# Kernel optimization log

Measured on AMD Instinct MI355X. Metric: run time of the kernel, lower is better.

The kernel has to match this reference:

```python
import jax, jax.numpy as jnp
import numpy as np

NEG_SLOPE = 0.2
EPS = 1e-16


def _gat_layer(x, src, dst, W, a_src, a_dst, b, n_nodes):
    # x: [N, Fin], W: [Fout, Fin]; src/dst: [E'] (self-loops already appended)
    h = x @ W.T                              # [N, Fout]
    alpha_s = h @ a_src                      # [N] per-source score
    alpha_d = h @ a_dst                      # [N] per-dest score
    e = jax.nn.leaky_relu(alpha_s[src] + alpha_d[dst], NEG_SLOPE)  # [E']
    # segment softmax over destination nodes (PyG softmax semantics)
    m = jax.ops.segment_max(e, dst, num_segments=n_nodes)          # [N]
    ex = jnp.exp(e - m[dst])                                       # [E']
    s = jax.ops.segment_sum(ex, dst, num_segments=n_nodes)         # [N]
    alpha = ex / (s[dst] + EPS)                                    # [E']
    out = jax.ops.segment_sum(alpha[:, None] * h[src], dst, num_segments=n_nodes)
    return out + b, alpha


def setup_inputs() -> dict:
    key = jax.random.key(0)
    ks = jax.random.split(key, 14)
    N, E, F_IN, H1, H2, F_OUT = 50000, 800000, 128, 64, 64, 32
    sc = 0.1
    return {
        "x": jax.random.normal(ks[0], (N, F_IN), dtype=jnp.float32),
        "edge_index": jax.random.randint(ks[1], (2, E), 0, N, dtype=jnp.int64),
        "W1": jax.random.normal(ks[2], (H1, F_IN), dtype=jnp.float32) * sc,
        "a_src1": jax.random.normal(ks[3], (H1,), dtype=jnp.float32) * sc,
        "a_dst1": jax.random.normal(ks[4], (H1,), dtype=jnp.float32) * sc,
        "b1": jnp.zeros((H1,), dtype=jnp.float32),
        "W2": jax.random.normal(ks[5], (H2, H1), dtype=jnp.float32) * sc,
        "a_src2": jax.random.normal(ks[6], (H2,), dtype=jnp.float32) * sc,
        "a_dst2": jax.random.normal(ks[7], (H2,), dtype=jnp.float32) * sc,
        "b2": jnp.zeros((H2,), dtype=jnp.float32),
        "W3": jax.random.normal(ks[8], (F_OUT, H2), dtype=jnp.float32) * sc,
        "a_src3": jax.random.normal(ks[9], (F_OUT,), dtype=jnp.float32) * sc,
        "a_dst3": jax.random.normal(ks[10], (F_OUT,), dtype=jnp.float32) * sc,
        "b3": jnp.zeros((F_OUT,), dtype=jnp.float32),
    }


def reference(x, edge_index, W1, a_src1, a_dst1, b1, W2, a_src2, a_dst2, b2, W3, a_src3, a_dst3, b3):
    N = x.shape[0]
    loops = jnp.arange(N, dtype=edge_index.dtype)
    src = jnp.concatenate([edge_index[0], loops])  # add_self_loops=True
    dst = jnp.concatenate([edge_index[1], loops])

    h, alpha1 = _gat_layer(x, src, dst, W1, a_src1, a_dst1, b1, N)
    h = jax.nn.relu(h)
    h, _ = _gat_layer(h, src, dst, W2, a_src2, a_dst2, b2, N)
    h = jax.nn.relu(h)
    out, _ = _gat_layer(h, src, dst, W3, a_src3, a_dst3, b3, N)
    # att_tuple = (edge_index with self loops, attention coefficients of layer 1)
    return (jnp.stack([src, dst]), alpha1, out)
```

## Files before the change

kernel.cpp:

```cpp
#include <hip/hip_runtime.h>
#include <hip/hip_bf16.h>
#include <math.h>

#define NEG_SLOPE 0.2f
#define GAT_EPS 1e-16f

constexpr int NN = 50000;
constexpr int NE = 800000;
constexpr int EP = NE + NN;
constexpr int NB = (NN + 255) / 256;

__device__ inline void edge_sd(const int* __restrict__ ei, int i, int& s, int& d) {
    if (i < NE) { s = ei[i]; d = ei[NE + i]; }
    else        { s = d = i - NE; }
}

__device__ inline float bflo(unsigned int h) { return __uint_as_float(h << 16); }
__device__ inline float bfhi(unsigned int h) { return __uint_as_float(h & 0xffff0000u); }

__global__ void k_edges_hist(const int* __restrict__ ei, float* __restrict__ out0,
                             unsigned int* __restrict__ cntp,
                             unsigned short* __restrict__ rank) {
    int i = blockIdx.x * blockDim.x + threadIdx.x;
    if (i >= EP) return;
    int s, d; edge_sd(ei, i, s, d);
    __builtin_nontemporal_store((float)s, &out0[i]);
    __builtin_nontemporal_store((float)d, &out0[EP + i]);
    unsigned int add = (d & 1) ? 0x10000u : 1u;
    unsigned int old = atomicAdd(&cntp[d >> 1], add);
    unsigned short r = (unsigned short)((d & 1) ? (old >> 16) : (old & 0xffffu));
    __builtin_nontemporal_store(r, &rank[i]);
}

__global__ void k_scan1(const unsigned int* __restrict__ cntp, int* __restrict__ rowptr,
                        int* __restrict__ bsum) {
    __shared__ int sh[256];
    int t = threadIdx.x, i = blockIdx.x * 256 + t;
    int v = 0;
    if (i < NN) {
        unsigned int pv = cntp[i >> 1];
        v = (i & 1) ? (int)(pv >> 16) : (int)(pv & 0xffffu);
    }
    sh[t] = v; __syncthreads();
    for (int off = 1; off < 256; off <<= 1) {
        int x = (t >= off) ? sh[t - off] : 0;
        __syncthreads();
        sh[t] += x;
        __syncthreads();
    }
    if (i < NN) rowptr[i] = sh[t] - v;
    if (t == 255) bsum[blockIdx.x] = sh[255];
}

__global__ void k_scan2(int* __restrict__ bsum, int* __restrict__ boff) {
    __shared__ int sh[256];
    int t = threadIdx.x;
    int v = (t < NB) ? bsum[t] : 0;
    sh[t] = v; __syncthreads();
    for (int off = 1; off < 256; off <<= 1) {
        int x = (t >= off) ? sh[t - off] : 0;
        __syncthreads();
        sh[t] += x;
        __syncthreads();
    }
    if (t < NB) boff[t] = sh[t] - v;
}

__global__ void k_scan3(int* __restrict__ rowptr, const int* __restrict__ boff) {
    int i = blockIdx.x * blockDim.x + threadIdx.x;
    if (i < NN) rowptr[i] += boff[i >> 8];
    if (i == 0) rowptr[NN] = EP;
}

__global__ void k_fill(const int* __restrict__ ei, const unsigned short* __restrict__ rank,
                       const int* __restrict__ rowptr, unsigned short* __restrict__ col) {
    int i = blockIdx.x * blockDim.x + threadIdx.x;
    if (i >= EP) return;
    int s, d; edge_sd(ei, i, s, d);
    int pos = rowptr[d] + (int)rank[i];
    col[pos] = (unsigned short)s;
}

__global__ void k_alpha_out(const int* __restrict__ ei, const float* __restrict__ as_,
                            const float* __restrict__ ad_, const float* __restrict__ inv,
                            float* __restrict__ out_alpha) {
    int i = blockIdx.x * blockDim.x + threadIdx.x;
    if (i >= EP) return;
    int s, d; edge_sd(ei, i, s, d);
    float v = as_[s] + ad_[d];
    v = v > 0.f ? v : NEG_SLOPE * v;
    __builtin_nontemporal_store(__expf(v) * inv[d], &out_alpha[i]);
}

struct alignas(8) bh4 { __hip_bfloat16 a, b, c, d; };

__device__ inline void fma4(float4& acc, float x, const float4& w) {
    acc.x = fmaf(x, w.x, acc.x);
    acc.y = fmaf(x, w.y, acc.y);
    acc.z = fmaf(x, w.z, acc.z);
    acc.w = fmaf(x, w.w, acc.w);
}

template <int FIN, int FOUT, int NPB>
__global__ __launch_bounds__(256) void k_gemm_t(const float* __restrict__ in,
                                                const float* __restrict__ W,
                                                const float* __restrict__ avs,
                                                const float* __restrict__ avd,
                                                __hip_bfloat16* __restrict__ H,
                                                float* __restrict__ as_,
                                                float* __restrict__ ad_, int n) {
    constexpr int TF = FOUT / 4;
    constexpr int XS = FIN + 4;
    constexpr int WS = FOUT + 4;
    __shared__ float sX[NPB * XS];
    __shared__ float sWt[FIN * WS];
    int tid = threadIdx.x;
    for (int idx = tid; idx < FIN * FOUT; idx += 256) {
        int f = idx % FOUT, k = idx / FOUT;
        sWt[k * WS + f] = W[f * FIN + k];
    }
    int nb = blockIdx.x * NPB;
    for (int idx = tid; idx < NPB * (FIN / 4); idx += 256) {
        int node = idx / (FIN / 4), kq = idx % (FIN / 4);
        int g = nb + node;
        float4 v = make_float4(0.f, 0.f, 0.f, 0.f);
        if (g < n) v = *(const float4*)&in[(size_t)g * FIN + kq * 4];
        *(float4*)&sX[node * XS + kq * 4] = v;
    }
    __syncthreads();

    int fq = tid % TF, ng = tid / TF;
    int n0 = ng * 4;
    float4 acc0 = make_float4(0.f, 0.f, 0.f, 0.f);
    float4 acc1 = acc0, acc2 = acc0, acc3 = acc0;
    for (int k = 0; k < FIN; k += 4) {
        float4 w0 = *(const float4*)&sWt[(k + 0) * WS + fq * 4];
        float4 w1 = *(const float4*)&sWt[(k + 1) * WS + fq * 4];
        float4 w2 = *(const float4*)&sWt[(k + 2) * WS + fq * 4];
        float4 w3 = *(const float4*)&sWt[(k + 3) * WS + fq * 4];
        float4 x0 = *(const float4*)&sX[(n0 + 0) * XS + k];
        float4 x1 = *(const float4*)&sX[(n0 + 1) * XS + k];
        float4 x2 = *(const float4*)&sX[(n0 + 2) * XS + k];
        float4 x3 = *(const float4*)&sX[(n0 + 3) * XS + k];
        fma4(acc0, x0.x, w0); fma4(acc0, x0.y, w1); fma4(acc0, x0.z, w2); fma4(acc0, x0.w, w3);
        fma4(acc1, x1.x, w0); fma4(acc1, x1.y, w1); fma4(acc1, x1.z, w2); fma4(acc1, x1.w, w3);
        fma4(acc2, x2.x, w0); fma4(acc2, x2.y, w1); fma4(acc2, x2.z, w2); fma4(acc2, x2.w, w3);
        fma4(acc3, x3.x, w0); fma4(acc3, x3.y, w1); fma4(acc3, x3.z, w2); fma4(acc3, x3.w, w3);
    }
    float4 accs[4] = {acc0, acc1, acc2, acc3};
    float4 vs4 = *(const float4*)&avs[fq * 4];
    float4 vd4 = *(const float4*)&avd[fq * 4];
#pragma unroll
    for (int j = 0; j < 4; ++j) {
        int g = nb + n0 + j;
        float ps = accs[j].x * vs4.x + accs[j].y * vs4.y + accs[j].z * vs4.z + accs[j].w * vs4.w;
        float pd = accs[j].x * vd4.x + accs[j].y * vd4.y + accs[j].z * vd4.z + accs[j].w * vd4.w;
#pragma unroll
        for (int off = TF / 2; off; off >>= 1) {
            ps += __shfl_down(ps, off, TF);
            pd += __shfl_down(pd, off, TF);
        }
        if (g < n) {
            if (fq == 0) { as_[g] = ps; ad_[g] = pd; }
            bh4 o;
            o.a = __float2bfloat16(accs[j].x);
            o.b = __float2bfloat16(accs[j].y);
            o.c = __float2bfloat16(accs[j].z);
            o.d = __float2bfloat16(accs[j].w);
            *(bh4*)&H[(size_t)g * FOUT + fq * 4] = o;
        }
    }
}

template <int FOUT, bool RELU, bool WRITE_INV>
__global__ __launch_bounds__(256) void k_node_attn(
    const int* __restrict__ rowptr, const unsigned short* __restrict__ col,
    const float* __restrict__ as_, const float* __restrict__ ad_,
    const __hip_bfloat16* __restrict__ H, const float* __restrict__ bias,
    float* __restrict__ outp, float* __restrict__ inv_out) {
    int wid = (blockIdx.x * blockDim.x + threadIdx.x) >> 6;
    int lane = threadIdx.x & 63;
    if (wid >= NN) return;
    int start = rowptr[wid], end = rowptr[wid + 1];
    float adv = ad_[wid];
    const unsigned int* __restrict__ H2 = (const unsigned int*)H;

    float sloc = 0.f;
    float ax = 0.f, ay = 0.f;
    for (int c = start; c < end; c += 64) {
        int e = c + lane;
        float p = 0.f;
        int sc = 0;
        if (e < end) {
            sc = (int)col[e];
            float v = as_[sc] + adv;
            v = v > 0.f ? v : NEG_SLOPE * v;
            p = __expf(v);
        }
        sloc += p;
        int cnt = end - c; if (cnt > 64) cnt = 64;
        if (FOUT == 64) {
            int half = lane >> 5, fl = lane & 31;
            int j = 0;
            for (; j + 8 <= cnt; j += 8) {
                int e0 = j + half, e1 = j + 2 + half, e2 = j + 4 + half, e3 = j + 6 + half;
                float p0 = __shfl(p, e0), p1 = __shfl(p, e1);
                float p2 = __shfl(p, e2), p3 = __shfl(p, e3);
                int s0 = __shfl(sc, e0), s1 = __shfl(sc, e1);
                int s2 = __shfl(sc, e2), s3 = __shfl(sc, e3);
                unsigned int h0 = H2[((size_t)s0 << 5) + fl];
                unsigned int h1 = H2[((size_t)s1 << 5) + fl];
                unsigned int h2 = H2[((size_t)s2 << 5) + fl];
                unsigned int h3 = H2[((size_t)s3 << 5) + fl];
                ax = fmaf(p0, bflo(h0), ax); ay = fmaf(p0, bfhi(h0), ay);
                ax = fmaf(p1, bflo(h1), ax); ay = fmaf(p1, bfhi(h1), ay);
                ax = fmaf(p2, bflo(h2), ax); ay = fmaf(p2, bfhi(h2), ay);
                ax = fmaf(p3, bflo(h3), ax); ay = fmaf(p3, bfhi(h3), ay);
            }
            for (; j < cnt; j += 2) {
                int e0 = j + half;
                float p0 = __shfl(p, e0);
                int   s0 = __shfl(sc, e0);
                unsigned int h0 = H2[((size_t)s0 << 5) + fl];
                ax = fmaf(p0, bflo(h0), ax); ay = fmaf(p0, bfhi(h0), ay);
            }
        } else {
            int q = lane >> 4, fl = lane & 15;
            int j = 0;
            for (; j + 16 <= cnt; j += 16) {
                int e0 = j + q, e1 = j + 4 + q, e2 = j + 8 + q, e3 = j + 12 + q;
                float p0 = __shfl(p, e0), p1 = __shfl(p, e1);
                float p2 = __shfl(p, e2), p3 = __shfl(p, e3);
                int s0 = __shfl(sc, e0), s1 = __shfl(sc, e1);
                int s2 = __shfl(sc, e2), s3 = __shfl(sc, e3);
                unsigned int h0 = H2[((size_t)s0 << 4) + fl];
                unsigned int h1 = H2[((size_t)s1 << 4) + fl];
                unsigned int h2 = H2[((size_t)s2 << 4) + fl];
                unsigned int h3 = H2[((size_t)s3 << 4) + fl];
                ax = fmaf(p0, bflo(h0), ax); ay = fmaf(p0, bfhi(h0), ay);
                ax = fmaf(p1, bflo(h1), ax); ay = fmaf(p1, bfhi(h1), ay);
                ax = fmaf(p2, bflo(h2), ax); ay = fmaf(p2, bfhi(h2), ay);
                ax = fmaf(p3, bflo(h3), ax); ay = fmaf(p3, bfhi(h3), ay);
            }
            for (; j < cnt; j += 4) {
                int e0 = j + q;
                float p0 = __shfl(p, e0);
                int   s0 = __shfl(sc, e0);
                unsigned int h0 = H2[((size_t)s0 << 4) + fl];
                ax = fmaf(p0, bflo(h0), ax); ay = fmaf(p0, bfhi(h0), ay);
            }
        }
    }
    for (int off = 32; off; off >>= 1) sloc += __shfl_xor(sloc, off);
    float inv = 1.f / (sloc + GAT_EPS);
    if (WRITE_INV && lane == 0) inv_out[wid] = inv;

    if (FOUT == 64) {
        ax += __shfl_xor(ax, 32);
        ay += __shfl_xor(ay, 32);
        if (lane < 32) {
            float2 bb = *(const float2*)&bias[lane * 2];
            float o0 = bb.x + ax * inv;
            float o1 = bb.y + ay * inv;
            if (RELU) { o0 = fmaxf(o0, 0.f); o1 = fmaxf(o1, 0.f); }
            *(float2*)&outp[((size_t)wid << 6) + lane * 2] = make_float2(o0, o1);
        }
    } else {
        ax += __shfl_xor(ax, 32); ay += __shfl_xor(ay, 32);
        ax += __shfl_xor(ax, 16); ay += __shfl_xor(ay, 16);
        if (lane < 16) {
            float2 bb = *(const float2*)&bias[lane * 2];
            float o0 = bb.x + ax * inv;
            float o1 = bb.y + ay * inv;
            if (RELU) { o0 = fmaxf(o0, 0.f); o1 = fmaxf(o1, 0.f); }
            *(float2*)&outp[((size_t)wid << 5) + lane * 2] = make_float2(o0, o1);
        }
    }
}

extern "C" void kernel_launch(void* const* d_in, const int* in_sizes, int n_in,
                              void* d_out, int out_size, void* d_ws, size_t ws_size,
                              hipStream_t stream) {
    const float* x  = (const float*)d_in[0];
    const int*   ei = (const int*)d_in[1];
    const float* W1 = (const float*)d_in[2];
    const float* as1 = (const float*)d_in[3];
    const float* ad1 = (const float*)d_in[4];
    const float* b1 = (const float*)d_in[5];
    const float* W2 = (const float*)d_in[6];
    const float* as2 = (const float*)d_in[7];
    const float* ad2 = (const float*)d_in[8];
    const float* b2 = (const float*)d_in[9];
    const float* W3 = (const float*)d_in[10];
    const float* as3 = (const float*)d_in[11];
    const float* ad3 = (const float*)d_in[12];
    const float* b3 = (const float*)d_in[13];

    float* out = (float*)d_out;
    float* out_edges = out;
    float* out_alpha = out + 2 * EP;
    float* out_final = out + 3 * EP;

    char* w = (char*)d_ws;
    size_t o = 0;
    float* as_ = (float*)(w + o); o += (size_t)NN * 4;
    float* ad_ = (float*)(w + o); o += (size_t)NN * 4;
    float* inv = (float*)(w + o); o += (size_t)NN * 4;
    __hip_bfloat16* H = (__hip_bfloat16*)(w + o); o += (size_t)NN * 64 * 2;
    int* rowptr = (int*)(w + o); o += ((size_t)(NN + 1) * 4 + 15) & ~15ull;
    unsigned int* cntp = (unsigned int*)(w + o); o += (size_t)(NN / 2) * 4;
    unsigned short* rank = (unsigned short*)(w + o); o += (size_t)EP * 2;
    unsigned short* col  = (unsigned short*)(w + o); o += (size_t)EP * 2;
    int* bsum   = (int*)(w + o); o += 1024;
    int* boff   = (int*)(w + o); o += 1024;
    const size_t aggBytes = (size_t)NN * 64 * 4;
    float* agg = (ws_size >= o + aggBytes)
        ? (float*)(w + o)
        : (float*)d_in[0];

    hipMemsetAsync(cntp, 0, (size_t)(NN / 2) * 4, stream);
    k_edges_hist<<<(EP + 255) / 256, 256, 0, stream>>>(ei, out_edges, cntp, rank);
    k_scan1<<<NB, 256, 0, stream>>>(cntp, rowptr, bsum);
    k_scan2<<<1, 256, 0, stream>>>(bsum, boff);
    k_scan3<<<NB, 256, 0, stream>>>(rowptr, boff);
    k_fill<<<(EP + 255) / 256, 256, 0, stream>>>(ei, rank, rowptr, col);

    const int nblk = (NN * 64 + 255) / 256;

    k_gemm_t<128, 64, 64><<<(NN + 63) / 64, 256, 0, stream>>>(x, W1, as1, ad1, H, as_, ad_, NN);
    k_node_attn<64, true, true><<<nblk, 256, 0, stream>>>(rowptr, col, as_, ad_, H, b1,
                                                          agg, inv);
    k_alpha_out<<<(EP + 255) / 256, 256, 0, stream>>>(ei, as_, ad_, inv, out_alpha);

    k_gemm_t<64, 64, 64><<<(NN + 63) / 64, 256, 0, stream>>>(agg, W2, as2, ad2, H, as_, ad_, NN);
    k_node_attn<64, true, false><<<nblk, 256, 0, stream>>>(rowptr, col, as_, ad_, H, b2,
                                                           agg, nullptr);

    k_gemm_t<64, 32, 128><<<(NN + 127) / 128, 256, 0, stream>>>(agg, W3, as3, ad3, H, as_, ad_,
                                                                NN);
    k_node_attn<32, false, false><<<nblk, 256, 0, stream>>>(rowptr, col, as_, ad_, H, b3,
                                                            out_final, nullptr);
}
```

Measured before the change: 316.5 us.

## Partition CSR histogram and fill by destination slice per XCD group

The histogram and fill kernels are rewritten so that each of 8 block groups (selected by blockIdx & 7, which likely maps to the XCDs) handles only destinations in its own node slice. All groups scan every edge, but atomics stay local to one slice, which should keep the atomic targets in that XCD's L2. The per-edge rank array is dropped, and fill now claims slots with atomicAdd on a per-node cursor. The cost is that every group rereads the full edge list, and the order of neighbours within a row is no longer deterministic, which can change float summation order.

Measured after the change: 341.4 us. 7.9% more time.

```diff
diff --git a/kernel.cpp b/kernel.cpp
--- a/kernel.cpp
+++ b/kernel.cpp
@@ -9,6 +9,10 @@
 constexpr int NE = 800000;
 constexpr int EP = NE + NN;
 constexpr int NB = (NN + 255) / 256;
+constexpr int SLICE = 6250;
+constexpr int HG = 416;
+constexpr int HSTRIDE = HG * 256;
+constexpr int OCHUNK = (EP + 7) / 8;
 
 __device__ inline void edge_sd(const int* __restrict__ ei, int i, int& s, int& d) {
     if (i < NE) { s = ei[i]; d = ei[NE + i]; }
@@ -18,18 +22,22 @@
 __device__ inline float bflo(unsigned int h) { return __uint_as_float(h << 16); }
 __device__ inline float bfhi(unsigned int h) { return __uint_as_float(h & 0xffff0000u); }
 
-__global__ void k_edges_hist(const int* __restrict__ ei, float* __restrict__ out0,
-                             unsigned int* __restrict__ cntp,
-                             unsigned short* __restrict__ rank) {
-    int i = blockIdx.x * blockDim.x + threadIdx.x;
-    if (i >= EP) return;
-    int s, d; edge_sd(ei, i, s, d);
-    __builtin_nontemporal_store((float)s, &out0[i]);
-    __builtin_nontemporal_store((float)d, &out0[EP + i]);
-    unsigned int add = (d & 1) ? 0x10000u : 1u;
-    unsigned int old = atomicAdd(&cntp[d >> 1], add);
-    unsigned short r = (unsigned short)((d & 1) ? (old >> 16) : (old & 0xffffu));
-    __builtin_nontemporal_store(r, &rank[i]);
+__global__ void k_hist_x(const int* __restrict__ ei, float* __restrict__ out0,
+                         unsigned int* __restrict__ cntp) {
+    int g = blockIdx.x & 7;
+    int bi = blockIdx.x >> 3;
+    for (int i = bi * 256 + threadIdx.x; i < EP; i += HSTRIDE) {
+        int d = (i < NE) ? ei[NE + i] : i - NE;
+        if (i / OCHUNK == g) {
+            int s = (i < NE) ? ei[i] : i - NE;
+            __builtin_nontemporal_store((float)s, &out0[i]);
+            __builtin_nontemporal_store((float)d, &out0[EP + i]);
+        }
+        if ((unsigned)d / (unsigned)SLICE == (unsigned)g) {
+            unsigned int add = (d & 1) ? 0x10000u : 1u;
+            atomicAdd(&cntp[d >> 1], add);
+        }
+    }
 }
 
 __global__ void k_scan1(const unsigned int* __restrict__ cntp, int* __restrict__ rowptr,
@@ -66,19 +74,29 @@
     if (t < NB) boff[t] = sh[t] - v;
 }
 
-__global__ void k_scan3(int* __restrict__ rowptr, const int* __restrict__ boff) {
+__global__ void k_scan3(int* __restrict__ rowptr, const int* __restrict__ boff,
+                        int* __restrict__ cur) {
     int i = blockIdx.x * blockDim.x + threadIdx.x;
-    if (i < NN) rowptr[i] += boff[i >> 8];
+    if (i < NN) {
+        int r = rowptr[i] + boff[i >> 8];
+        rowptr[i] = r;
+        cur[i] = r;
+    }
     if (i == 0) rowptr[NN] = EP;
 }
 
-__global__ void k_fill(const int* __restrict__ ei, const unsigned short* __restrict__ rank,
-                       const int* __restrict__ rowptr, unsigned short* __restrict__ col) {
-    int i = blockIdx.x * blockDim.x + threadIdx.x;
-    if (i >= EP) return;
-    int s, d; edge_sd(ei, i, s, d);
-    int pos = rowptr[d] + (int)rank[i];
-    col[pos] = (unsigned short)s;
+__global__ void k_fill_x(const int* __restrict__ ei, int* __restrict__ cur,
+                         unsigned short* __restrict__ col) {
+    int g = blockIdx.x & 7;
+    int bi = blockIdx.x >> 3;
+    for (int i = bi * 256 + threadIdx.x; i < EP; i += HSTRIDE) {
+        int d = (i < NE) ? ei[NE + i] : i - NE;
+        if ((unsigned)d / (unsigned)SLICE == (unsigned)g) {
+            int s = (i < NE) ? ei[i] : i - NE;
+            int pos = atomicAdd(&cur[d], 1);
+            col[pos] = (unsigned short)s;
+        }
+    }
 }
 
 __global__ void k_alpha_out(const int* __restrict__ ei, const float* __restrict__ as_,
@@ -309,8 +327,8 @@
     __hip_bfloat16* H = (__hip_bfloat16*)(w + o); o += (size_t)NN * 64 * 2;
     int* rowptr = (int*)(w + o); o += ((size_t)(NN + 1) * 4 + 15) & ~15ull;
     unsigned int* cntp = (unsigned int*)(w + o); o += (size_t)(NN / 2) * 4;
-    unsigned short* rank = (unsigned short*)(w + o); o += (size_t)EP * 2;
-    unsigned short* col  = (unsigned short*)(w + o); o += (size_t)EP * 2;
+    int* cur    = (int*)(w + o); o += (size_t)NN * 4;
+    unsigned short* col = (unsigned short*)(w + o); o += (size_t)EP * 2;
     int* bsum   = (int*)(w + o); o += 1024;
     int* boff   = (int*)(w + o); o += 1024;
     const size_t aggBytes = (size_t)NN * 64 * 4;
@@ -319,11 +337,11 @@
         : (float*)d_in[0];
 
     hipMemsetAsync(cntp, 0, (size_t)(NN / 2) * 4, stream);
-    k_edges_hist<<<(EP + 255) / 256, 256, 0, stream>>>(ei, out_edges, cntp, rank);
+    k_hist_x<<<8 * HG, 256, 0, stream>>>(ei, out_edges, cntp);
     k_scan1<<<NB, 256, 0, stream>>>(cntp, rowptr, bsum);
     k_scan2<<<1, 256, 0, stream>>>(bsum, boff);
-    k_scan3<<<NB, 256, 0, stream>>>(rowptr, boff);
-    k_fill<<<(EP + 255) / 256, 256, 0, stream>>>(ei, rank, rowptr, col);
+    k_scan3<<<NB, 256, 0, stream>>>(rowptr, boff, cur);
+    k_fill_x<<<8 * HG, 256, 0, stream>>>(ei, cur, col);
 
     const int nblk = (NN * 64 + 255) / 256;
 
```
